# Performance work log

Measured on AMD Instinct MI355X. Metric: run time of the kernel, lower is better.

The kernel has to match this reference:

```python
import jax, jax.numpy as jnp
import numpy as np

N = 100000   # nodes
E = 1600000  # edges
D = 128      # input_dim
H = 128      # hidden_dim
L = 3        # n_layers
G = 512      # graphs in batch
OUT = 64     # latent_dim
BN_EPS = 1e-5
SLOPE = 0.2  # LeakyReLU negative slope


def setup_inputs() -> dict:
    key = jax.random.key(0)
    ks = jax.random.split(key, 13)
    s = 1.0 / np.sqrt(H)
    return {
        "x": jax.random.normal(ks[0], (N, D), jnp.float32),
        "edge_index": jax.random.randint(ks[1], (2, E), 0, N),
        "batch": jnp.sort(jax.random.randint(ks[2], (N,), 0, G)),
        # stacked GINConv MLP params (input_dim == hidden_dim so all layers stack)
        "W1s": jax.random.normal(ks[3], (L, D, H), jnp.float32) * s,
        "b1s": jax.random.normal(ks[4], (L, H), jnp.float32) * 0.01,
        "g1s": jnp.ones((L, H), jnp.float32),
        "be1s": jnp.zeros((L, H), jnp.float32),
        "W2s": jax.random.normal(ks[5], (L, H, H), jnp.float32) * s,
        "b2s": jax.random.normal(ks[6], (L, H), jnp.float32) * 0.01,
        # final BN + FC
        "bn_g": jnp.ones((H,), jnp.float32),
        "bn_b": jnp.zeros((H,), jnp.float32),
        "fcW": jax.random.normal(ks[7], (H, OUT), jnp.float32) * s,
        "fcb": jax.random.normal(ks[8], (OUT,), jnp.float32) * 0.01,
    }


def _batchnorm(h, g, b):
    mu = jnp.mean(h, axis=0)
    var = jnp.var(h, axis=0)
    return (h - mu) * jax.lax.rsqrt(var + BN_EPS) * g + b


def _gin_layer(x, src, dst, W1, b1, g1, be1, W2, b2):
    # GINConv: (1+eps)*x + sum_{j in N(i)} x_j, eps=0; then MLP
    agg = jax.ops.segment_sum(x[src], dst, num_segments=N)
    h = x + agg
    h = jax.nn.leaky_relu(h @ W1 + b1, SLOPE)
    h = _batchnorm(h, g1, be1)
    h = jax.nn.leaky_relu(h @ W2 + b2, SLOPE)
    return h


def reference(x, edge_index, batch, W1s, b1s, g1s, be1s, W2s, b2s, bn_g, bn_b, fcW, fcb):
    src, dst = edge_index[0], edge_index[1]
    h = x
    for l in range(L):
        h = _gin_layer(h, src, dst, W1s[l], b1s[l], g1s[l], be1s[l], W2s[l], b2s[l])
        # dropout is identity in eval mode
    pooled = jax.ops.segment_sum(h, batch, num_segments=G)  # global_add_pool [G, H]
    out = _batchnorm(pooled, bn_g, bn_b)
    return out @ fcW + fcb
```

## Files before the change

kernel.cpp:

```cpp
#include <hip/hip_runtime.h>


typedef __attribute__((ext_vector_type(8))) __bf16 bf16x8;
typedef __attribute__((ext_vector_type(4))) float  f32x4;

__device__ __forceinline__ unsigned short f2bf(float f) {
    union { float f; unsigned int u; } v; v.f = f;
    unsigned int r = v.u + 0x7fffu + ((v.u >> 16) & 1u);
    return (unsigned short)(r >> 16);
}
__device__ __forceinline__ float bf2f(unsigned short h) {
    union { unsigned int u; float f; } v; v.u = ((unsigned int)h) << 16;
    return v.f;
}


__global__ void zero2_kernel(int* __restrict__ a, int* __restrict__ b, int n) {
    int i = blockIdx.x * 256 + threadIdx.x;
    if (i < n) { a[i] = 0; b[i] = 0; }
}

__global__ void hist_kernel(const int* __restrict__ dst, int* __restrict__ deg, int E) {
    int e = blockIdx.x * 256 + threadIdx.x;
    if (e < E) atomicAdd(&deg[dst[e]], 1);
}

__global__ void scan1_kernel(const int* __restrict__ deg, int* __restrict__ ofs,
                             int* __restrict__ bsum, int n) {
    __shared__ int sh[256];
    int tid = threadIdx.x;
    int i = blockIdx.x * 256 + tid;
    int v = (i < n) ? deg[i] : 0;
    sh[tid] = v;
    __syncthreads();
    for (int o = 1; o < 256; o <<= 1) {
        int tmp = (tid >= o) ? sh[tid - o] : 0;
        __syncthreads();
        sh[tid] += tmp;
        __syncthreads();
    }
    if (i < n) ofs[i] = sh[tid] - v;
    if (tid == 255) bsum[blockIdx.x] = sh[255];
}

__global__ void scan2_kernel(int* __restrict__ bsum, int nb) {
    __shared__ int sh[1024];
    int tid = threadIdx.x;
    int v = (tid < nb) ? bsum[tid] : 0;
    sh[tid] = v;
    __syncthreads();
    for (int o = 1; o < 1024; o <<= 1) {
        int tmp = (tid >= o) ? sh[tid - o] : 0;
        __syncthreads();
        sh[tid] += tmp;
        __syncthreads();
    }
    if (tid < nb) bsum[tid] = sh[tid] - v;
}

__global__ void scan3_kernel(int* __restrict__ ofs, const int* __restrict__ bsum,
                             int n, int Etot) {
    int i = blockIdx.x * 256 + threadIdx.x;
    if (i < n) ofs[i] += bsum[blockIdx.x];
    if (i == 0) ofs[n] = Etot;
}

__global__ void fill_kernel(const int* __restrict__ src, const int* __restrict__ dst,
                            const int* __restrict__ ofs, int* __restrict__ cur,
                            int* __restrict__ csr, int E) {
    int e = blockIdx.x * 256 + threadIdx.x;
    if (e >= E) return;
    int d = dst[e];
    int p = atomicAdd(&cur[d], 1);
    csr[ofs[d] + p] = src[e];
}


__global__ void prep_w1_all(const float* __restrict__ W1s, unsigned short* __restrict__ Bth,
                            unsigned short* __restrict__ Btl,
                            float* __restrict__ colsum, float* __restrict__ colsq,
                            int total, int nstats) {
    int t = blockIdx.x * 256 + threadIdx.x;
    if (t < nstats) { colsum[t] = 0.f; colsq[t] = 0.f; }
    if (t >= total) return;
    int lbase = t & ~16383;
    int r = t & 16383;
    int n = r >> 7, k = r & 127;
    float v = W1s[lbase + k * 128 + n];
    unsigned short h = f2bf(v);
    Bth[t] = h;
    Btl[t] = f2bf(v - bf2f(h));
}

__global__ void w2t_fold(const float* __restrict__ W2, const float* __restrict__ b2,
                         const float* __restrict__ g1, const float* __restrict__ be1,
                         const float* __restrict__ colsum, const float* __restrict__ colsq,
                         unsigned short* __restrict__ Bth, unsigned short* __restrict__ Btl,
                         float* __restrict__ b2p, int nrows) {
    __shared__ float s[128], tt[128];
    int tid = threadIdx.x;
    if (tid < 128) {
        float mu = colsum[tid] / (float)nrows;
        float var = colsq[tid] / (float)nrows - mu * mu;
        float rs = rsqrtf(var + 1e-5f);
        float sc = rs * g1[tid];
        s[tid] = sc;
        tt[tid] = be1[tid] - mu * sc;
    }
    __syncthreads();
    int t = blockIdx.x * 256 + tid;
    int n = t >> 7, k = t & 127;
    float v = s[k] * W2[k * 128 + n];
    unsigned short h = f2bf(v);
    Bth[t] = h;
    Btl[t] = f2bf(v - bf2f(h));
    if (blockIdx.x == 0) {
        __shared__ float part[2][128];
        int nn = tid & 127, half = tid >> 7;
        float acc = 0.f;
        for (int kk = half * 64; kk < half * 64 + 64; ++kk)
            acc += tt[kk] * W2[kk * 128 + nn];
        part[half][nn] = acc;
        __syncthreads();
        if (tid < 128) b2p[tid] = b2[tid] + part[0][tid] + part[1][tid];
    }
}


#define APAD 136

__launch_bounds__(512, 4)
__global__ void fused_agg_gemm1(const float* __restrict__ h, const int* __restrict__ ofs,
                                const int* __restrict__ csr,
                                const unsigned short* __restrict__ Bh,
                                const unsigned short* __restrict__ Bl,
                                const float* __restrict__ bias,
                                unsigned short* __restrict__ Ohi,
                                unsigned short* __restrict__ Olo,
                                float* __restrict__ colsum, float* __restrict__ colsq,
                                int n) {
    __shared__ unsigned short AhL[64][APAD];
    __shared__ unsigned short AlL[64][APAD];

    const int rowbase = blockIdx.x * 64;
    const int hw = threadIdx.x >> 5;
    const int lane = threadIdx.x & 31;
    const float4* base = (const float4*)h;

    for (int i = 0; i < 4; ++i) {
        int lrow = hw * 4 + i;
        int node = rowbase + lrow;
        float ax = 0.f, ay = 0.f, az = 0.f, aw = 0.f;
        if (node < n) {
            float4 a = base[node * 32 + lane];
            ax = a.x; ay = a.y; az = a.z; aw = a.w;
            int e0 = ofs[node], e1 = ofs[node + 1];
            int j = e0;
            for (; j + 8 <= e1; j += 8) {
                int s[8];
#pragma unroll
                for (int u = 0; u < 8; ++u) s[u] = csr[j + u];
                float4 v[8];
#pragma unroll
                for (int u = 0; u < 8; ++u) v[u] = base[s[u] * 32 + lane];
#pragma unroll
                for (int u = 0; u < 8; ++u) {
                    ax += v[u].x; ay += v[u].y; az += v[u].z; aw += v[u].w;
                }
            }
            for (; j + 4 <= e1; j += 4) {
                int s0 = csr[j], s1 = csr[j + 1], s2 = csr[j + 2], s3 = csr[j + 3];
                float4 v0 = base[s0 * 32 + lane];
                float4 v1 = base[s1 * 32 + lane];
                float4 v2 = base[s2 * 32 + lane];
                float4 v3 = base[s3 * 32 + lane];
                ax += (v0.x + v1.x) + (v2.x + v3.x);
                ay += (v0.y + v1.y) + (v2.y + v3.y);
                az += (v0.z + v1.z) + (v2.z + v3.z);
                aw += (v0.w + v1.w) + (v2.w + v3.w);
            }
            for (; j < e1; ++j) {
                float4 v = base[csr[j] * 32 + lane];
                ax += v.x; ay += v.y; az += v.z; aw += v.w;
            }
        }
        unsigned short h0 = f2bf(ax), h1 = f2bf(ay), h2 = f2bf(az), h3 = f2bf(aw);
        unsigned short l0 = f2bf(ax - bf2f(h0)), l1 = f2bf(ay - bf2f(h1));
        unsigned short l2 = f2bf(az - bf2f(h2)), l3 = f2bf(aw - bf2f(h3));
        ushort4 ph = {h0, h1, h2, h3};
        ushort4 pl = {l0, l1, l2, l3};
        *(ushort4*)(&AhL[lrow][lane * 4]) = ph;
        *(ushort4*)(&AlL[lrow][lane * 4]) = pl;
    }
    __syncthreads();

    const int lane64 = threadIdx.x & 63;
    const int wv = threadIdx.x >> 6;
    const int l15 = lane64 & 15;
    const int lg = lane64 >> 4;
    const int colbase = wv * 16;

    bf16x8 bh[4], bl[4];
#pragma unroll
    for (int ks = 0; ks < 4; ++ks) {
        int nn = colbase + l15;
        int k = ks * 32 + lg * 8;
        bh[ks] = *(const bf16x8*)(Bh + nn * 128 + k);
        bl[ks] = *(const bf16x8*)(Bl + nn * 128 + k);
    }
    float bias0 = bias[colbase + l15];
    float s0 = 0.f, q0 = 0.f;

#pragma unroll
    for (int mr = 0; mr < 4; ++mr) {
        int lrow = mr * 16 + l15;
        bf16x8 ah[4], al[4];
#pragma unroll
        for (int ks = 0; ks < 4; ++ks) {
            ah[ks] = *(const bf16x8*)(&AhL[lrow][ks * 32 + lg * 8]);
            al[ks] = *(const bf16x8*)(&AlL[lrow][ks * 32 + lg * 8]);
        }
        f32x4 acc = {0.f, 0.f, 0.f, 0.f};
#pragma unroll
        for (int ks = 0; ks < 4; ++ks) {
            acc = __builtin_amdgcn_mfma_f32_16x16x32_bf16(ah[ks], bh[ks], acc, 0, 0, 0);
            acc = __builtin_amdgcn_mfma_f32_16x16x32_bf16(ah[ks], bl[ks], acc, 0, 0, 0);
            acc = __builtin_amdgcn_mfma_f32_16x16x32_bf16(al[ks], bh[ks], acc, 0, 0, 0);
        }
        int orow0 = rowbase + mr * 16 + lg * 4;
#pragma unroll
        for (int r = 0; r < 4; ++r) {
            int orow = orow0 + r;
            if (orow < n) {
                float v0 = acc[r] + bias0;
                v0 = v0 > 0.f ? v0 : 0.2f * v0;
                int c0 = colbase + l15;
                unsigned short h0 = f2bf(v0);
                Ohi[orow * 128 + c0] = h0;
                Olo[orow * 128 + c0] = f2bf(v0 - bf2f(h0));
                s0 += v0; q0 += v0 * v0;
            }
        }
    }
    s0 += __shfl_xor(s0, 16); s0 += __shfl_xor(s0, 32);
    q0 += __shfl_xor(q0, 16); q0 += __shfl_xor(q0, 32);
    if (lg == 0) {
        atomicAdd(&colsum[colbase + l15], s0);
        atomicAdd(&colsq[colbase + l15], q0);
    }
}


__global__ void gemm2_split(const unsigned short* __restrict__ Ah, const unsigned short* __restrict__ Al,
                            const unsigned short* __restrict__ Bh, const unsigned short* __restrict__ Bl,
                            const float* __restrict__ bias, float* __restrict__ Of32,
                            int nrows) {
    const int lane = threadIdx.x & 63;
    const int wv = threadIdx.x >> 6;
    const int l15 = lane & 15;
    const int lg = lane >> 4;
    const int colbase = wv * 32;
    const int rowbase = blockIdx.x * 128;

    bf16x8 bh[2][4], bl[2][4];
#pragma unroll
    for (int nc = 0; nc < 2; ++nc)
#pragma unroll
        for (int ks = 0; ks < 4; ++ks) {
            int n = colbase + nc * 16 + l15;
            int k = ks * 32 + lg * 8;
            bh[nc][ks] = *(const bf16x8*)(Bh + n * 128 + k);
            bl[nc][ks] = *(const bf16x8*)(Bl + n * 128 + k);
        }
    float bias0 = bias[colbase + l15];
    float bias1 = bias[colbase + 16 + l15];

#pragma unroll 2
    for (int mr = 0; mr < 8; ++mr) {
        int arow = rowbase + mr * 16 + l15;
        int ar = (arow < nrows) ? arow : (nrows - 1);
        const unsigned short* pa = Ah + ar * 128 + lg * 8;
        const unsigned short* pl = Al + ar * 128 + lg * 8;
        bf16x8 ah[4], al[4];
#pragma unroll
        for (int ks = 0; ks < 4; ++ks) {
            ah[ks] = *(const bf16x8*)(pa + ks * 32);
            al[ks] = *(const bf16x8*)(pl + ks * 32);
        }
        f32x4 acc0 = {0.f, 0.f, 0.f, 0.f};
        f32x4 acc1 = {0.f, 0.f, 0.f, 0.f};
#pragma unroll
        for (int ks = 0; ks < 4; ++ks) {
            acc0 = __builtin_amdgcn_mfma_f32_16x16x32_bf16(ah[ks], bh[0][ks], acc0, 0, 0, 0);
            acc1 = __builtin_amdgcn_mfma_f32_16x16x32_bf16(ah[ks], bh[1][ks], acc1, 0, 0, 0);
            acc0 = __builtin_amdgcn_mfma_f32_16x16x32_bf16(ah[ks], bl[0][ks], acc0, 0, 0, 0);
            acc1 = __builtin_amdgcn_mfma_f32_16x16x32_bf16(ah[ks], bl[1][ks], acc1, 0, 0, 0);
            acc0 = __builtin_amdgcn_mfma_f32_16x16x32_bf16(al[ks], bh[0][ks], acc0, 0, 0, 0);
            acc1 = __builtin_amdgcn_mfma_f32_16x16x32_bf16(al[ks], bh[1][ks], acc1, 0, 0, 0);
        }
        int orow0 = rowbase + mr * 16 + lg * 4;
#pragma unroll
        for (int r = 0; r < 4; ++r) {
            int orow = orow0 + r;
            if (orow < nrows) {
                float v0 = acc0[r] + bias0;
                v0 = v0 > 0.f ? v0 : 0.2f * v0;
                float v1 = acc1[r] + bias1;
                v1 = v1 > 0.f ? v1 : 0.2f * v1;
                Of32[orow * 128 + colbase + l15] = v0;
                Of32[orow * 128 + colbase + 16 + l15] = v1;
            }
        }
    }
}


__global__ void graph_bounds(const int* __restrict__ batch, int* __restrict__ gstart,
                             int n, int G) {
    int i = blockIdx.x * 256 + threadIdx.x;
    if (i >= n) return;
    int b = batch[i];
    if (i == 0) {
        for (int x = 0; x <= b; ++x) gstart[x] = 0;
    } else {
        int p = batch[i - 1];
        for (int x = p + 1; x <= b; ++x) gstart[x] = i;
    }
    if (i == n - 1) {
        for (int x = b + 1; x <= G; ++x) gstart[x] = n;
    }
}

__global__ void pool_kernel(const float* __restrict__ h, const int* __restrict__ gstart,
                            float* __restrict__ pooled, int G) {
    int g = blockIdx.x * 8 + (threadIdx.x >> 5);
    if (g >= G) return;
    int lane = threadIdx.x & 31;
    const float4* base = (const float4*)h;
    float ax = 0.f, ay = 0.f, az = 0.f, aw = 0.f;
    int i0 = gstart[g], i1 = gstart[g + 1];
    for (int i = i0; i < i1; ++i) {
        float4 v = base[i * 32 + lane];
        ax += v.x; ay += v.y; az += v.z; aw += v.w;
    }
    float4 o = {ax, ay, az, aw};
    *(float4*)(pooled + g * 128 + lane * 4) = o;
}

__global__ void pool_stats(const float* __restrict__ pooled, const float* __restrict__ bn_g,
                           const float* __restrict__ bn_b, float* __restrict__ pscale,
                           float* __restrict__ pshift, int G) {
    __shared__ float ss[8][128], sq[8][128];
    int tid = threadIdx.x;
    int c = tid & 127, seg = tid >> 7;
    int per = (G + 7) / 8;
    int g0 = seg * per;
    int g1 = g0 + per; if (g1 > G) g1 = G;
    float s = 0.f, q = 0.f;
    for (int g = g0; g < g1; ++g) { float v = pooled[g * 128 + c]; s += v; q += v * v; }
    ss[seg][c] = s; sq[seg][c] = q;
    __syncthreads();
    if (seg == 0) {
        for (int t2 = 1; t2 < 8; ++t2) { s += ss[t2][c]; q += sq[t2][c]; }
        float mu = s / (float)G;
        float var = q / (float)G - mu * mu;
        float rs = rsqrtf(var + 1e-5f);
        float sc = rs * bn_g[c];
        pscale[c] = sc;
        pshift[c] = bn_b[c] - mu * sc;
    }
}

__global__ void final_fc(const float* __restrict__ pooled, const float* __restrict__ pscale,
                         const float* __restrict__ pshift, const float* __restrict__ fcW,
                         const float* __restrict__ fcb, float* __restrict__ out, int total) {
    int idx = blockIdx.x * 256 + threadIdx.x;
    if (idx >= total) return;
    int o = idx & 63, g = idx >> 6;
    float acc = fcb[o];
    const float* prow = pooled + g * 128;
#pragma unroll 4
    for (int c = 0; c < 128; ++c) {
        float z = prow[c] * pscale[c] + pshift[c];
        acc += z * fcW[c * 64 + o];
    }
    out[idx] = acc;
}


extern "C" void kernel_launch(void* const* d_in, const int* in_sizes, int n_in,
                              void* d_out, int out_size, void* d_ws, size_t ws_size,
                              hipStream_t stream) {
    const float* x    = (const float*)d_in[0];
    const int*   ei   = (const int*)d_in[1];
    const int*   batch= (const int*)d_in[2];
    const float* W1s  = (const float*)d_in[3];
    const float* b1s  = (const float*)d_in[4];
    const float* g1s  = (const float*)d_in[5];
    const float* be1s = (const float*)d_in[6];
    const float* W2s  = (const float*)d_in[7];
    const float* b2s  = (const float*)d_in[8];
    const float* bn_g = (const float*)d_in[9];
    const float* bn_b = (const float*)d_in[10];
    const float* fcW  = (const float*)d_in[11];
    const float* fcb  = (const float*)d_in[12];
    float* out = (float*)d_out;

    const int N = in_sizes[0] / 128;
    const int E = in_sizes[1] / 2;
    const int G = out_size / 64;
    const int L = in_sizes[3] / (128 * 128);
    const int* src = ei;
    const int* dst = ei + E;

    size_t off = 0;
    auto carve = [&](size_t bytes) -> void* {
        void* p = (char*)d_ws + off;
        off += (bytes + 255) & ~(size_t)255;
        return p;
    };
    int* deg    = (int*)carve((size_t)N * 4);
    int* cur    = (int*)carve((size_t)N * 4);
    int* ofs    = (int*)carve((size_t)(N + 1) * 4);
    int* bsum   = (int*)carve(4096 * 4);
    int* csr    = (int*)carve((size_t)E * 4);
    int* gstart = (int*)carve((size_t)(G + 1) * 4);
    unsigned short* h1H  = (unsigned short*)carve((size_t)N * 128 * 2);
    unsigned short* h1L  = (unsigned short*)carve((size_t)N * 128 * 2);
    float* hbuf  = (float*)carve((size_t)N * 128 * 4);
    unsigned short* wt1H = (unsigned short*)carve((size_t)L * 16384 * 2);
    unsigned short* wt1L = (unsigned short*)carve((size_t)L * 16384 * 2);
    unsigned short* wt2H = (unsigned short*)carve(16384 * 2);
    unsigned short* wt2L = (unsigned short*)carve(16384 * 2);
    float* b2p    = (float*)carve(128 * 4);
    float* colsum = (float*)carve((size_t)L * 128 * 4);
    float* colsq  = (float*)carve((size_t)L * 128 * 4);
    float* pooled = (float*)carve((size_t)G * 128 * 4);
    float* pscale = (float*)carve(128 * 4);
    float* pshift = (float*)carve(128 * 4);
    (void)ws_size; (void)n_in;

    int wtot = L * 16384;
    prep_w1_all<<<(wtot + 255) / 256, 256, 0, stream>>>(W1s, wt1H, wt1L,
                                                        colsum, colsq, wtot, L * 128);

    zero2_kernel<<<(N + 255) / 256, 256, 0, stream>>>(deg, cur, N);
    hist_kernel<<<(E + 255) / 256, 256, 0, stream>>>(dst, deg, E);
    int nb1 = (N + 255) / 256;
    scan1_kernel<<<nb1, 256, 0, stream>>>(deg, ofs, bsum, N);
    scan2_kernel<<<1, 1024, 0, stream>>>(bsum, nb1);
    scan3_kernel<<<nb1, 256, 0, stream>>>(ofs, bsum, N, E);
    fill_kernel<<<(E + 255) / 256, 256, 0, stream>>>(src, dst, ofs, cur, csr, E);

    const float* hprev = x;
    int fusedBlocks = (N + 63) / 64;
    int gemmBlocks = (N + 127) / 128;
    for (int l = 0; l < L; ++l) {
        fused_agg_gemm1<<<fusedBlocks, 512, 0, stream>>>(hprev, ofs, csr,
                                                         wt1H + l * 16384, wt1L + l * 16384,
                                                         b1s + l * 128,
                                                         h1H, h1L,
                                                         colsum + l * 128, colsq + l * 128, N);
        w2t_fold<<<64, 256, 0, stream>>>(W2s + (size_t)l * 16384, b2s + l * 128,
                                         g1s + l * 128, be1s + l * 128,
                                         colsum + l * 128, colsq + l * 128,
                                         wt2H, wt2L, b2p, N);
        gemm2_split<<<gemmBlocks, 256, 0, stream>>>(h1H, h1L, wt2H, wt2L, b2p, hbuf, N);
        hprev = hbuf;
    }

    graph_bounds<<<(N + 255) / 256, 256, 0, stream>>>(batch, gstart, N, G);
    pool_kernel<<<(G + 7) / 8, 256, 0, stream>>>(hbuf, gstart, pooled, G);
    pool_stats<<<1, 1024, 0, stream>>>(pooled, bn_g, bn_b, pscale, pshift, G);
    final_fc<<<(G * 64 + 255) / 256, 256, 0, stream>>>(pooled, pscale, pshift, fcW, fcb,
                                                       out, G * 64);
}
```

Measured before the change: 952.8 us.

## Stage gemm2 A tiles in LDS with 64-row blocks and raise occupancy bounds

New measurement: 876.2 us. 1.09x faster.

```diff
diff --git a/kernel.cpp b/kernel.cpp
--- a/kernel.cpp
+++ b/kernel.cpp
@@ -129,7 +129,7 @@
 
 #define APAD 136
 
-__launch_bounds__(512, 4)
+__launch_bounds__(512, 8)
 __global__ void fused_agg_gemm1(const float* __restrict__ h, const int* __restrict__ ofs,
                                 const int* __restrict__ csr,
                                 const unsigned short* __restrict__ Bh,
@@ -251,64 +251,69 @@
 }
 
 
+__launch_bounds__(512, 8)
 __global__ void gemm2_split(const unsigned short* __restrict__ Ah, const unsigned short* __restrict__ Al,
                             const unsigned short* __restrict__ Bh, const unsigned short* __restrict__ Bl,
                             const float* __restrict__ bias, float* __restrict__ Of32,
                             int nrows) {
-    const int lane = threadIdx.x & 63;
+    __shared__ unsigned short AhL[64][APAD];
+    __shared__ unsigned short AlL[64][APAD];
+
+    const int rowbase = blockIdx.x * 64;
+
+    int t = threadIdx.x;
+#pragma unroll
+    for (int c = 0; c < 2; ++c) {
+        int chunk = c * 512 + t;
+        int row = chunk >> 4;
+        int seg = chunk & 15;
+        int gr = rowbase + row;
+        int gsrc = (gr < nrows ? gr : nrows - 1) * 128 + seg * 8;
+        *(uint4*)(&AhL[row][seg * 8]) = *(const uint4*)(Ah + gsrc);
+        *(uint4*)(&AlL[row][seg * 8]) = *(const uint4*)(Al + gsrc);
+    }
+    __syncthreads();
+
+    const int lane64 = threadIdx.x & 63;
     const int wv = threadIdx.x >> 6;
-    const int l15 = lane & 15;
-    const int lg = lane >> 4;
-    const int colbase = wv * 32;
-    const int rowbase = blockIdx.x * 128;
-
-    bf16x8 bh[2][4], bl[2][4];
-#pragma unroll
-    for (int nc = 0; nc < 2; ++nc)
+    const int l15 = lane64 & 15;
+    const int lg = lane64 >> 4;
+    const int colbase = wv * 16;
+
+    bf16x8 bh[4], bl[4];
+#pragma unroll
+    for (int ks = 0; ks < 4; ++ks) {
+        int nn = colbase + l15;
+        int k = ks * 32 + lg * 8;
+        bh[ks] = *(const bf16x8*)(Bh + nn * 128 + k);
+        bl[ks] = *(const bf16x8*)(Bl + nn * 128 + k);
+    }
+    float bias0 = bias[colbase + l15];
+
+#pragma unroll
+    for (int mr = 0; mr < 4; ++mr) {
+        int lrow = mr * 16 + l15;
+        bf16x8 ah[4], al[4];
 #pragma unroll
         for (int ks = 0; ks < 4; ++ks) {
-            int n = colbase + nc * 16 + l15;
-            int k = ks * 32 + lg * 8;
-            bh[nc][ks] = *(const bf16x8*)(Bh + n * 128 + k);
-            bl[nc][ks] = *(const bf16x8*)(Bl + n * 128 + k);
-        }
-    float bias0 = bias[colbase + l15];
-    float bias1 = bias[colbase + 16 + l15];
-
-#pragma unroll 2
-    for (int mr = 0; mr < 8; ++mr) {
-        int arow = rowbase + mr * 16 + l15;
-        int ar = (arow < nrows) ? arow : (nrows - 1);
-        const unsigned short* pa = Ah + ar * 128 + lg * 8;
-        const unsigned short* pl = Al + ar * 128 + lg * 8;
-        bf16x8 ah[4], al[4];
+            ah[ks] = *(const bf16x8*)(&AhL[lrow][ks * 32 + lg * 8]);
+            al[ks] = *(const bf16x8*)(&AlL[lrow][ks * 32 + lg * 8]);
+        }
+        f32x4 acc = {0.f, 0.f, 0.f, 0.f};
 #pragma unroll
         for (int ks = 0; ks < 4; ++ks) {
-            ah[ks] = *(const bf16x8*)(pa + ks * 32);
-            al[ks] = *(const bf16x8*)(pl + ks * 32);
-        }
-        f32x4 acc0 = {0.f, 0.f, 0.f, 0.f};
-        f32x4 acc1 = {0.f, 0.f, 0.f, 0.f};
-#pragma unroll
-        for (int ks = 0; ks < 4; ++ks) {
-            acc0 = __builtin_amdgcn_mfma_f32_16x16x32_bf16(ah[ks], bh[0][ks], acc0, 0, 0, 0);
-            acc1 = __builtin_amdgcn_mfma_f32_16x16x32_bf16(ah[ks], bh[1][ks], acc1, 0, 0, 0);
-            acc0 = __builtin_amdgcn_mfma_f32_16x16x32_bf16(ah[ks], bl[0][ks], acc0, 0, 0, 0);
-            acc1 = __builtin_amdgcn_mfma_f32_16x16x32_bf16(ah[ks], bl[1][ks], acc1, 0, 0, 0);
-            acc0 = __builtin_amdgcn_mfma_f32_16x16x32_bf16(al[ks], bh[0][ks], acc0, 0, 0, 0);
-            acc1 = __builtin_amdgcn_mfma_f32_16x16x32_bf16(al[ks], bh[1][ks], acc1, 0, 0, 0);
+            acc = __builtin_amdgcn_mfma_f32_16x16x32_bf16(ah[ks], bh[ks], acc, 0, 0, 0);
+            acc = __builtin_amdgcn_mfma_f32_16x16x32_bf16(ah[ks], bl[ks], acc, 0, 0, 0);
+            acc = __builtin_amdgcn_mfma_f32_16x16x32_bf16(al[ks], bh[ks], acc, 0, 0, 0);
         }
         int orow0 = rowbase + mr * 16 + lg * 4;
 #pragma unroll
         for (int r = 0; r < 4; ++r) {
             int orow = orow0 + r;
             if (orow < nrows) {
-                float v0 = acc0[r] + bias0;
+                float v0 = acc[r] + bias0;
                 v0 = v0 > 0.f ? v0 : 0.2f * v0;
-                float v1 = acc1[r] + bias1;
-                v1 = v1 > 0.f ? v1 : 0.2f * v1;
                 Of32[orow * 128 + colbase + l15] = v0;
-                Of32[orow * 128 + colbase + 16 + l15] = v1;
             }
         }
     }
@@ -453,19 +458,18 @@
     fill_kernel<<<(E + 255) / 256, 256, 0, stream>>>(src, dst, ofs, cur, csr, E);
 
     const float* hprev = x;
-    int fusedBlocks = (N + 63) / 64;
-    int gemmBlocks = (N + 127) / 128;
+    int tileBlocks = (N + 63) / 64;
     for (int l = 0; l < L; ++l) {
-        fused_agg_gemm1<<<fusedBlocks, 512, 0, stream>>>(hprev, ofs, csr,
-                                                         wt1H + l * 16384, wt1L + l * 16384,
-                                                         b1s + l * 128,
-                                                         h1H, h1L,
-                                                         colsum + l * 128, colsq + l * 128, N);
+        fused_agg_gemm1<<<tileBlocks, 512, 0, stream>>>(hprev, ofs, csr,
+                                                        wt1H + l * 16384, wt1L + l * 16384,
+                                                        b1s + l * 128,
+                                                        h1H, h1L,
+                                                        colsum + l * 128, colsq + l * 128, N);
         w2t_fold<<<64, 256, 0, stream>>>(W2s + (size_t)l * 16384, b2s + l * 128,
                                          g1s + l * 128, be1s + l * 128,
                                          colsum + l * 128, colsq + l * 128,
                                          wt2H, wt2L, b2p, N);
-        gemm2_split<<<gemmBlocks, 256, 0, stream>>>(h1H, h1L, wt2H, wt2L, b2p, hbuf, N);
+        gemm2_split<<<tileBlocks, 512, 0, stream>>>(h1H, h1L, wt2H, wt2L, b2p, hbuf, N);
         hprev = hbuf;
     }
 
```
